# Kernel optimization log

Measured on AMD Instinct MI355X. Metric: run time of the kernel, lower is better.

Reference implementation:

```python
import jax, jax.numpy as jnp
import numpy as np

N_NODES = 50000
N_EDGES = 600000
D = 128


def setup_inputs() -> dict:
    key = jax.random.key(0)
    k1, k2, k3 = jax.random.split(key, 3)
    x = jax.random.normal(k1, (N_NODES, D), dtype=jnp.float32)
    # Glorot-like init for the GCN linear weight
    W = jax.random.normal(k2, (D, D), dtype=jnp.float32) * (1.0 / np.sqrt(D))
    b = jnp.zeros((D,), dtype=jnp.float32)
    edge_index = jax.random.randint(k3, (2, N_EDGES), 0, N_NODES, dtype=jnp.int64)
    edge_attr = jnp.zeros((N_EDGES,), dtype=jnp.float32)   # unused by this layer
    batch = jnp.zeros((N_NODES,), dtype=jnp.int64)          # unused by this layer
    y = jnp.zeros((N_NODES,), dtype=jnp.int64)              # unused by this layer
    return {"x": x, "W": W, "b": b, "edge_index": edge_index,
            "edge_attr": edge_attr, "batch": batch, "y": y}


def reference(x, W, b, edge_index, edge_attr, batch, y):
    # GCNConv with default add_self_loops=True, symmetric normalization,
    # followed by ReLU (dropout disabled since GNNdrop == 0).
    N = x.shape[0]
    self_loops = jnp.arange(N, dtype=edge_index.dtype)
    src = jnp.concatenate([edge_index[0], self_loops])  # [E+N]
    dst = jnp.concatenate([edge_index[1], self_loops])  # [E+N]

    # Degree over destination nodes (includes self-loops)
    ones = jnp.ones(src.shape[0], dtype=x.dtype)
    deg = jax.ops.segment_sum(ones, dst, num_segments=N)          # [N]
    dinv = jnp.where(deg > 0, jax.lax.rsqrt(deg), 0.0)            # deg^{-1/2}
    norm = dinv[src] * dinv[dst]                                   # [E+N]

    # Linear transform first (as PyG GCNConv does), then gather-scale-scatter
    h = x @ W                                                      # [N, D]
    msg = h[src] * norm[:, None]                                   # [E+N, D]
    out = jax.ops.segment_sum(msg, dst, num_segments=N) + b       # [N, D]
    return jax.nn.relu(out)
```

## Files before the change

### kernel.cpp

```cpp
#include <hip/hip_runtime.h>

#define D 128
#define NBH 256
#define CAP 4096

typedef __attribute__((ext_vector_type(8))) short bf16x8;
typedef __attribute__((ext_vector_type(4))) float f32x4;
typedef __attribute__((ext_vector_type(8))) unsigned short us8;
typedef __attribute__((ext_vector_type(4))) int i32x4;

static __device__ __forceinline__ float bf2f(unsigned short u) {
    union { unsigned int i; float f; } c; c.i = ((unsigned int)u) << 16; return c.f;
}
static __device__ __forceinline__ unsigned short f2bf(float f) {
    union { float f; unsigned int i; } c; c.f = f;
    unsigned int r = c.i + 0x7FFFu + ((c.i >> 16) & 1u);
    return (unsigned short)(r >> 16);
}

__global__ __launch_bounds__(256) void k_wprep(const float* __restrict__ W,
                                               unsigned short* __restrict__ Wt) {
    int t = (int)blockIdx.x * 256 + (int)threadIdx.x;
    int k = t >> 7, c = t & 127;
    Wt[c * D + k] = f2bf(W[t]);
}

__global__ __launch_bounds__(256) void k_gemm_hist(const float* __restrict__ x,
                                                   const unsigned short* __restrict__ Wt,
                                                   const int* __restrict__ dst,
                                                   int* __restrict__ counts2d,
                                                   unsigned short* __restrict__ hs,
                                                   int N, int E, int nbuck) {
    if ((int)blockIdx.x < NBH) {
        __shared__ int bins[1024];
        for (int t = threadIdx.x; t < nbuck; t += 256) bins[t] = 0;
        __syncthreads();
        const int k = (int)blockIdx.x;
        const long long stride = (long long)NBH * 1024;
        for (long long i = ((long long)k * 256 + threadIdx.x) * 4; i < E; i += stride) {
            if (i + 4 <= E) {
                i32x4 d = *(const i32x4*)(dst + i);
                atomicAdd(&bins[d.x >> 6], 1);
                atomicAdd(&bins[d.y >> 6], 1);
                atomicAdd(&bins[d.z >> 6], 1);
                atomicAdd(&bins[d.w >> 6], 1);
            } else {
                for (long long j = i; j < E; ++j) atomicAdd(&bins[dst[j] >> 6], 1);
            }
        }
        __syncthreads();
        for (int t = threadIdx.x; t < nbuck; t += 256)
            counts2d[t * NBH + k] = bins[t];
        return;
    }

    const int wave = threadIdx.x >> 6;
    const int l    = threadIdx.x & 63;
    const int m0   = ((int)blockIdx.x - NBH) * 64 + wave * 16;
    const int lr   = l & 15;
    const int kg   = l >> 4;
    const int row_a = m0 + lr;

    f32x4 acc[8];
#pragma unroll
    for (int t = 0; t < 8; ++t) acc[t] = (f32x4){0.f, 0.f, 0.f, 0.f};

#pragma unroll
    for (int kk = 0; kk < 4; ++kk) {
        const int kbase = kk * 32 + kg * 8;
        bf16x8 afrag;
        if (row_a < N) {
            const float* xp = x + (size_t)row_a * D + kbase;
            f32x4 x0 = *(const f32x4*)xp;
            f32x4 x1 = *(const f32x4*)(xp + 4);
#pragma unroll
            for (int j = 0; j < 4; ++j) afrag[j] = (short)f2bf(x0[j]);
#pragma unroll
            for (int j = 0; j < 4; ++j) afrag[4 + j] = (short)f2bf(x1[j]);
        } else {
#pragma unroll
            for (int j = 0; j < 8; ++j) afrag[j] = 0;
        }
#pragma unroll
        for (int nt = 0; nt < 8; ++nt) {
            bf16x8 bfrag = *(const bf16x8*)(Wt + (size_t)(nt * 16 + lr) * D + kbase);
            acc[nt] = __builtin_amdgcn_mfma_f32_16x16x32_bf16(afrag, bfrag, acc[nt], 0, 0, 0);
        }
    }

#pragma unroll
    for (int j = 0; j < 4; ++j) {
        int row = m0 + kg * 4 + j;
        if (row < N) {
#pragma unroll
            for (int nt = 0; nt < 8; ++nt)
                hs[(size_t)row * D + nt * 16 + lr] = f2bf(acc[nt][j]);
        }
    }
}

__global__ __launch_bounds__(256) void k_colscan(int* __restrict__ counts2d,
                                                 int* __restrict__ btot) {
    __shared__ int ts[256];
    const int b = (int)blockIdx.x;
    const int t = (int)threadIdx.x;
    int c = counts2d[b * NBH + t];
    ts[t] = c;
    __syncthreads();
    for (int off = 1; off < 256; off <<= 1) {
        int v = (t >= off) ? ts[t - off] : 0;
        __syncthreads();
        ts[t] += v;
        __syncthreads();
    }
    counts2d[b * NBH + t] = ts[t] - c;
    if (t == 255) btot[b] = ts[255];
}

__global__ __launch_bounds__(256) void k_scatter(const int* __restrict__ src,
                                                 const int* __restrict__ dst,
                                                 const int* __restrict__ btot,
                                                 const int* __restrict__ counts2d,
                                                 int* __restrict__ offsets,
                                                 unsigned int* __restrict__ sorted,
                                                 int E, int nbuck) {
    __shared__ int pref[1025];
    __shared__ int ts[256];
    __shared__ int base_l[1024];
    __shared__ int cur[1024];

    {
        const int t = (int)threadIdx.x;
        int e[4];
        int s = 0;
#pragma unroll
        for (int j = 0; j < 4; ++j) {
            int idx = t * 4 + j;
            int v = (idx < nbuck) ? btot[idx] : 0;
            e[j] = s;
            s += v;
        }
        ts[t] = s;
        __syncthreads();
        for (int off = 1; off < 256; off <<= 1) {
            int v = (t >= off) ? ts[t - off] : 0;
            __syncthreads();
            ts[t] += v;
            __syncthreads();
        }
        int base = ts[t] - s;
#pragma unroll
        for (int j = 0; j < 4; ++j) {
            int idx = t * 4 + j;
            if (idx <= 1024) pref[idx] = base + e[j];
        }
        if (t == 255) pref[1024] = ts[255];
        __syncthreads();
        for (int idx = t; idx <= nbuck; idx += 256)
            offsets[idx] = pref[idx];
    }

    const int k = (int)blockIdx.x;
    for (int t = threadIdx.x; t < nbuck; t += 256) {
        base_l[t] = pref[t] + counts2d[t * NBH + k];
        cur[t] = 0;
    }
    __syncthreads();

    const long long stride = (long long)NBH * 1024;
    for (long long i = ((long long)k * 256 + threadIdx.x) * 4; i < E; i += stride) {
        if (i + 4 <= E) {
            i32x4 d = *(const i32x4*)(dst + i);
            i32x4 s = *(const i32x4*)(src + i);
            int p;
            p = base_l[d.x >> 6] + atomicAdd(&cur[d.x >> 6], 1);
            sorted[p] = (unsigned int)(s.x & 0xFFFF) | ((unsigned int)(d.x & 63) << 16);
            p = base_l[d.y >> 6] + atomicAdd(&cur[d.y >> 6], 1);
            sorted[p] = (unsigned int)(s.y & 0xFFFF) | ((unsigned int)(d.y & 63) << 16);
            p = base_l[d.z >> 6] + atomicAdd(&cur[d.z >> 6], 1);
            sorted[p] = (unsigned int)(s.z & 0xFFFF) | ((unsigned int)(d.z & 63) << 16);
            p = base_l[d.w >> 6] + atomicAdd(&cur[d.w >> 6], 1);
            sorted[p] = (unsigned int)(s.w & 0xFFFF) | ((unsigned int)(d.w & 63) << 16);
        } else {
            for (long long j = i; j < E; ++j) {
                int dd = dst[j], ss = src[j];
                int p = base_l[dd >> 6] + atomicAdd(&cur[dd >> 6], 1);
                sorted[p] = (unsigned int)(ss & 0xFFFF) | ((unsigned int)(dd & 63) << 16);
            }
        }
    }
}

__global__ __launch_bounds__(256) void k_dinv(const unsigned int* __restrict__ sorted,
                                              const int* __restrict__ offsets,
                                              float* __restrict__ dinv, int N) {
    __shared__ int bins[64];
    const int b = (int)blockIdx.x;
    if (threadIdx.x < 64) bins[threadIdx.x] = 0;
    __syncthreads();
    const int off = offsets[b];
    const int cnt = offsets[b + 1] - off;
    for (int i = threadIdx.x; i < cnt; i += 256)
        atomicAdd(&bins[(sorted[off + i] >> 16) & 63], 1);
    __syncthreads();
    if (threadIdx.x < 64) {
        int v = b * 64 + (int)threadIdx.x;
        if (v < N) dinv[v] = rsqrtf((float)(bins[threadIdx.x] + 1));
    }
}

__global__ __launch_bounds__(512) void k_aggregate(const unsigned short* __restrict__ hs,
                                                   const unsigned int* __restrict__ sorted,
                                                   const int* __restrict__ offsets,
                                                   const float* __restrict__ dinv,
                                                   const float* __restrict__ bias,
                                                   float* __restrict__ out, int N) {
    __shared__ unsigned short srt[CAP];
    __shared__ int bins[64];
    __shared__ int boff[64];
    __shared__ int cur[64];

    const int bb  = (int)blockIdx.x;
    const int off = offsets[bb];
    const int cnt = offsets[bb + 1] - off;
    const bool fits = (cnt <= CAP);

    if (fits) {
        if (threadIdx.x < 64) bins[threadIdx.x] = 0;
        __syncthreads();
        for (int i = threadIdx.x; i < cnt; i += 512)
            atomicAdd(&bins[(sorted[off + i] >> 16) & 63], 1);
        __syncthreads();
        if (threadIdx.x < 64) {
            const int lane = (int)threadIdx.x;
            int bv = bins[lane];
            int inc = bv;
            for (int o = 1; o < 64; o <<= 1) {
                int t = __shfl_up(inc, o, 64);
                if (lane >= o) inc += t;
            }
            boff[lane] = inc - bv;
            cur[lane] = 0;
        }
        __syncthreads();
        for (int i = threadIdx.x; i < cnt; i += 512) {
            unsigned int e = sorted[off + i];
            int dl = (int)((e >> 16) & 63u);
            int p = boff[dl] + atomicAdd(&cur[dl], 1);
            srt[p] = (unsigned short)(e & 0xFFFFu);
        }
        __syncthreads();
    }

    const int grp  = (int)(threadIdx.x >> 4);
    const int lane = (int)(threadIdx.x & 15);
    const f32x4 b0 = *(const f32x4*)(bias + lane * 8);
    const f32x4 b1 = *(const f32x4*)(bias + lane * 8 + 4);

    for (int pass = 0; pass < 2; ++pass) {
        const int vl = pass * 32 + grp;
        const int v  = bb * 64 + vl;
        if (v >= N) continue;

        const float dv = dinv[v];
        float acc[8];
        {
            us8 h = *(const us8*)(hs + (size_t)v * D + lane * 8);
#pragma unroll
            for (int j = 0; j < 8; ++j) acc[j] = bf2f(h[j]) * dv;
        }

        if (fits) {
            int i   = boff[vl];
            int end = i + bins[vl];
            for (; i + 4 <= end; i += 4) {
                int s0 = srt[i + 0];
                int s1 = srt[i + 1];
                int s2 = srt[i + 2];
                int s3 = srt[i + 3];
                float d0 = dinv[s0], d1 = dinv[s1], d2 = dinv[s2], d3 = dinv[s3];
                us8 m0 = *(const us8*)(hs + (size_t)s0 * D + lane * 8);
                us8 m1 = *(const us8*)(hs + (size_t)s1 * D + lane * 8);
                us8 m2 = *(const us8*)(hs + (size_t)s2 * D + lane * 8);
                us8 m3 = *(const us8*)(hs + (size_t)s3 * D + lane * 8);
#pragma unroll
                for (int j = 0; j < 8; ++j)
                    acc[j] += (bf2f(m0[j]) * d0 + bf2f(m1[j]) * d1)
                            + (bf2f(m2[j]) * d2 + bf2f(m3[j]) * d3);
            }
            for (; i < end; ++i) {
                int s = srt[i];
                float ds = dinv[s];
                us8 m = *(const us8*)(hs + (size_t)s * D + lane * 8);
#pragma unroll
                for (int j = 0; j < 8; ++j) acc[j] += bf2f(m[j]) * ds;
            }
        } else {
            for (int i = 0; i < cnt; ++i) {
                unsigned int e = sorted[off + i];
                if ((int)((e >> 16) & 63u) == vl) {
                    int s = (int)(e & 0xFFFFu);
                    float ds = dinv[s];
                    us8 m = *(const us8*)(hs + (size_t)s * D + lane * 8);
#pragma unroll
                    for (int j = 0; j < 8; ++j) acc[j] += bf2f(m[j]) * ds;
                }
            }
        }

        f32x4 o0, o1;
#pragma unroll
        for (int j = 0; j < 4; ++j) {
            o0[j] = fmaxf(fmaf(acc[j],     dv, b0[j]), 0.0f);
            o1[j] = fmaxf(fmaf(acc[4 + j], dv, b1[j]), 0.0f);
        }
        float* op = out + (size_t)v * D + lane * 8;
        *(f32x4*)op       = o0;
        *(f32x4*)(op + 4) = o1;
    }
}

static inline char* align_up(char* p, size_t a) {
    return (char*)(((uintptr_t)p + a - 1) & ~(uintptr_t)(a - 1));
}

extern "C" void kernel_launch(void* const* d_in, const int* in_sizes, int n_in,
                              void* d_out, int out_size, void* d_ws, size_t ws_size,
                              hipStream_t stream) {
    const float* x  = (const float*)d_in[0];
    const float* W  = (const float*)d_in[1];
    const float* b  = (const float*)d_in[2];
    const int*   ei = (const int*)d_in[3];

    const int N = in_sizes[0] / D;
    const int E = in_sizes[3] / 2;
    const int* src = ei;
    const int* dst = ei + E;

    const int nbuck = (N + 63) >> 6;

    char* p = (char*)d_ws;
    int* counts2d        = (int*)p;            p = align_up(p + sizeof(int) * nbuck * NBH, 64);
    int* btot            = (int*)p;            p = align_up(p + sizeof(int) * nbuck, 64);
    int* offsets         = (int*)p;            p = align_up(p + sizeof(int) * (nbuck + 1), 64);
    unsigned int* sorted = (unsigned int*)p;   p = align_up(p + sizeof(unsigned int) * E, 64);
    float* dinv          = (float*)p;          p = align_up(p + sizeof(float) * N, 64);
    unsigned short* Wt   = (unsigned short*)p; p = align_up(p + sizeof(short) * D * D, 64);
    unsigned short* hs   = (unsigned short*)p;

    float* out = (float*)d_out;

    const int gemm_blks = (N + 63) / 64;

    k_wprep<<<(D * D) / 256, 256, 0, stream>>>(W, Wt);
    k_gemm_hist<<<NBH + gemm_blks, 256, 0, stream>>>(x, Wt, dst, counts2d, hs, N, E, nbuck);
    k_colscan<<<nbuck, 256, 0, stream>>>(counts2d, btot);
    k_scatter<<<NBH, 256, 0, stream>>>(src, dst, btot, counts2d, offsets, sorted, E, nbuck);
    k_dinv<<<nbuck, 256, 0, stream>>>(sorted, offsets, dinv, N);
    k_aggregate<<<nbuck, 512, 0, stream>>>(hs, sorted, offsets, dinv, b, out, N);
}
```

Before: 83.69 us.

## Assign one wavefront per destination node and split edges across four subgroups

The aggregation phase now maps each 64-lane wavefront to a single destination node, with four 16-lane subgroups striding through that node's edge list and combining partial sums via cross-lane shuffles. Before, each 16-lane group walked one node's full edge list with a 4-way unrolled loop. The aim is to even out per-wave load imbalance across nodes with different degrees and to expose more independent gathers per wave. The cost is extra shuffle reductions, idle lanes on low-degree nodes, and only one lane group issuing the final store. The prefix-sum store guard is also dropped, which is safe only if idx never exceeds 1024.

```diff
diff --git a/kernel.cpp b/kernel.cpp
--- a/kernel.cpp
+++ b/kernel.cpp
@@ -152,7 +152,7 @@
 #pragma unroll
         for (int j = 0; j < 4; ++j) {
             int idx = t * 4 + j;
-            if (idx <= 1024) pref[idx] = base + e[j];
+            pref[idx] = base + e[j];
         }
         if (t == 255) pref[1024] = ts[255];
         __syncthreads();
@@ -252,71 +252,79 @@
         __syncthreads();
     }
 
-    const int grp  = (int)(threadIdx.x >> 4);
-    const int lane = (int)(threadIdx.x & 15);
-    const f32x4 b0 = *(const f32x4*)(bias + lane * 8);
-    const f32x4 b1 = *(const f32x4*)(bias + lane * 8 + 4);
-
-    for (int pass = 0; pass < 2; ++pass) {
-        const int vl = pass * 32 + grp;
+    const int wv   = (int)(threadIdx.x >> 6);
+    const int lane = (int)(threadIdx.x & 63);
+    const int g    = lane >> 4;
+    const int sl   = lane & 15;
+    const f32x4 b0 = *(const f32x4*)(bias + sl * 8);
+    const f32x4 b1 = *(const f32x4*)(bias + sl * 8 + 4);
+
+    for (int t = 0; t < 8; ++t) {
+        const int vl = t * 8 + wv;
         const int v  = bb * 64 + vl;
         if (v >= N) continue;
 
         const float dv = dinv[v];
         float acc[8];
-        {
-            us8 h = *(const us8*)(hs + (size_t)v * D + lane * 8);
+        if (g == 0) {
+            us8 h = *(const us8*)(hs + (size_t)v * D + sl * 8);
 #pragma unroll
             for (int j = 0; j < 8; ++j) acc[j] = bf2f(h[j]) * dv;
+        } else {
+#pragma unroll
+            for (int j = 0; j < 8; ++j) acc[j] = 0.f;
         }
 
         if (fits) {
-            int i   = boff[vl];
-            int end = i + bins[vl];
-            for (; i + 4 <= end; i += 4) {
-                int s0 = srt[i + 0];
-                int s1 = srt[i + 1];
-                int s2 = srt[i + 2];
-                int s3 = srt[i + 3];
-                float d0 = dinv[s0], d1 = dinv[s1], d2 = dinv[s2], d3 = dinv[s3];
-                us8 m0 = *(const us8*)(hs + (size_t)s0 * D + lane * 8);
-                us8 m1 = *(const us8*)(hs + (size_t)s1 * D + lane * 8);
-                us8 m2 = *(const us8*)(hs + (size_t)s2 * D + lane * 8);
-                us8 m3 = *(const us8*)(hs + (size_t)s3 * D + lane * 8);
+            int i   = boff[vl] + g;
+            int end = boff[vl] + bins[vl];
+            for (; i + 4 < end; i += 8) {
+                int s0 = srt[i];
+                int s1 = srt[i + 4];
+                float d0 = dinv[s0], d1 = dinv[s1];
+                us8 m0 = *(const us8*)(hs + (size_t)s0 * D + sl * 8);
+                us8 m1 = *(const us8*)(hs + (size_t)s1 * D + sl * 8);
 #pragma unroll
                 for (int j = 0; j < 8; ++j)
-                    acc[j] += (bf2f(m0[j]) * d0 + bf2f(m1[j]) * d1)
-                            + (bf2f(m2[j]) * d2 + bf2f(m3[j]) * d3);
-            }
-            for (; i < end; ++i) {
+                    acc[j] += bf2f(m0[j]) * d0 + bf2f(m1[j]) * d1;
+            }
+            if (i < end) {
                 int s = srt[i];
                 float ds = dinv[s];
-                us8 m = *(const us8*)(hs + (size_t)s * D + lane * 8);
+                us8 m = *(const us8*)(hs + (size_t)s * D + sl * 8);
 #pragma unroll
                 for (int j = 0; j < 8; ++j) acc[j] += bf2f(m[j]) * ds;
             }
         } else {
-            for (int i = 0; i < cnt; ++i) {
+            for (int i = g; i < cnt; i += 4) {
                 unsigned int e = sorted[off + i];
                 if ((int)((e >> 16) & 63u) == vl) {
                     int s = (int)(e & 0xFFFFu);
                     float ds = dinv[s];
-                    us8 m = *(const us8*)(hs + (size_t)s * D + lane * 8);
+                    us8 m = *(const us8*)(hs + (size_t)s * D + sl * 8);
 #pragma unroll
                     for (int j = 0; j < 8; ++j) acc[j] += bf2f(m[j]) * ds;
                 }
             }
         }
 
-        f32x4 o0, o1;
-#pragma unroll
-        for (int j = 0; j < 4; ++j) {
-            o0[j] = fmaxf(fmaf(acc[j],     dv, b0[j]), 0.0f);
-            o1[j] = fmaxf(fmaf(acc[4 + j], dv, b1[j]), 0.0f);
-        }
-        float* op = out + (size_t)v * D + lane * 8;
-        *(f32x4*)op       = o0;
-        *(f32x4*)(op + 4) = o1;
+#pragma unroll
+        for (int j = 0; j < 8; ++j) {
+            acc[j] += __shfl_xor(acc[j], 16, 64);
+            acc[j] += __shfl_xor(acc[j], 32, 64);
+        }
+
+        if (g == 0) {
+            f32x4 o0, o1;
+#pragma unroll
+            for (int j = 0; j < 4; ++j) {
+                o0[j] = fmaxf(fmaf(acc[j],     dv, b0[j]), 0.0f);
+                o1[j] = fmaxf(fmaf(acc[4 + j], dv, b1[j]), 0.0f);
+            }
+            float* op = out + (size_t)v * D + sl * 8;
+            *(f32x4*)op       = o0;
+            *(f32x4*)(op + 4) = o1;
+        }
     }
 }
 
```

New measurement: 85.96 us. 1.03x slower.
